# Performance work log

Measured on AMD Instinct MI355X. Metric: run time of the kernel, lower is better.

Reference implementation:

```python
import jax, jax.numpy as jnp
import numpy as np

VOCAB = 50257
HIDDEN = 2048
BATCH = 8
SEQ = 2048
TOPK = 256


def setup_inputs() -> dict:
    key = jax.random.key(0)
    k1, k2 = jax.random.split(key)
    input_ids = jax.random.randint(k1, (BATCH, SEQ), 0, VOCAB, dtype=jnp.int64)
    W = jax.random.normal(k2, (VOCAB, HIDDEN), dtype=jnp.float32)
    return {"input_ids": input_ids, "W": W, "k": TOPK}


def reference(input_ids, W, k):
    # Embedding gather: [B, S] ids -> [B, S, H] logits (irregular row gather).
    logits = jnp.take(W, input_ids, axis=0)
    # Top-k over the last (hidden) dim, sorted descending (matches torch.topk).
    values, indices = jax.lax.top_k(logits, k)
    return values, indices.astype(jnp.int32)
```

## Files before the change

### kernel.cpp

```cpp
#include <hip/hip_runtime.h>
#include <stdint.h>

#define VOCAB  50257
#define HIDDEN 2048
#define NTOK   (8 * 2048)
#define TOPK   256
#define WPB    4


__device__ __forceinline__ void cmpex(uint64_t& a, uint64_t& b, bool desc) {
    bool gt = a > b;
    uint64_t mx = gt ? a : b;
    uint64_t mn = gt ? b : a;
    a = desc ? mx : mn;
    b = desc ? mn : mx;
}

__device__ __forceinline__ void step_xor(uint64_t& v, int r, int lane, int lx, int k) {
    uint64_t p = __shfl_xor(v, lx, 64);
    int i = lane * 4 + r;
    bool desc = ((i & k) == 0);
    bool low  = ((lane & lx) == 0);
    bool keep_max = (desc == low);
    bool gt = v > p;
    v = (keep_max == gt) ? v : p;
}

__global__ __launch_bounds__(256) void topk_kernel(
    const int* __restrict__ ids,
    const float* __restrict__ W,
    float* __restrict__ out)
{
    const int lane = threadIdx.x & 63;
    const int w    = threadIdx.x >> 6;
    const int row  = blockIdx.x * WPB + w;

    __shared__ __align__(16) uint64_t sel[WPB][256];

    const int id = ids[row];
    const float4* src = (const float4*)(W + (size_t)id * HIDDEN);

    uint32_t sv[32];
#pragma unroll
    for (int c = 0; c < 8; ++c) {
        float4 v = src[c * 64 + lane];
        uint32_t u[4] = {__float_as_uint(v.x), __float_as_uint(v.y),
                         __float_as_uint(v.z), __float_as_uint(v.w)};
#pragma unroll
        for (int j = 0; j < 4; ++j) {
            uint32_t m = (u[j] & 0x80000000u) ? 0xFFFFFFFFu : 0x80000000u;
            sv[c * 4 + j] = u[j] ^ m;
        }
    }

    auto count_ge = [&](uint32_t T) -> uint32_t {
        uint32_t tot = 0;
#pragma unroll
        for (int e = 0; e < 32; ++e)
            tot += (uint32_t)__popcll(__ballot(sv[e] >= T));
        return tot;
    };

    uint32_t lo = 0u, hi = 0xFFFFFFFFu;
    uint32_t Tsel = 0u;
    bool exact = false;
    while (lo < hi) {
        uint32_t mid = lo + ((hi - lo) >> 1) + 1u;
        uint32_t c = count_ge(mid);
        if (c == TOPK) { Tsel = mid; exact = true; break; }
        if (c > TOPK) lo = mid; else hi = mid - 1u;
    }

    uint32_t selmask = 0u;
    if (exact) {
#pragma unroll
        for (int e = 0; e < 32; ++e)
            if (sv[e] >= Tsel) selmask |= (1u << e);
    } else {
        uint32_t vstar = lo;
        uint32_t m = (vstar == 0xFFFFFFFFu) ? 0u : count_ge(vstar + 1u);
        uint32_t r = TOPK - m;
        const uint64_t below = (1ull << lane) - 1ull;
        uint32_t base = 0u;
        for (int c = 0; c < 8; ++c) {
            uint64_t bj[4];
            uint32_t pre = 0u;
#pragma unroll
            for (int j = 0; j < 4; ++j) {
                bj[j] = __ballot(sv[c * 4 + j] == vstar);
                pre += (uint32_t)__popcll(bj[j] & below);
            }
            uint32_t ownpref = 0u;
#pragma unroll
            for (int j = 0; j < 4; ++j) {
                int e = c * 4 + j;
                bool eq = (sv[e] == vstar);
                uint32_t rank = base + pre + ownpref;
                if (sv[e] > vstar || (eq && rank < r)) selmask |= (1u << e);
                ownpref += eq ? 1u : 0u;
            }
#pragma unroll
            for (int j = 0; j < 4; ++j)
                base += (uint32_t)__popcll(bj[j]);
        }
    }

    const uint64_t below = (1ull << lane) - 1ull;
    uint32_t pbase = 0u;
#pragma unroll
    for (int e = 0; e < 32; ++e) {
        bool s = (selmask >> e) & 1u;
        uint64_t mm = __ballot(s);
        if (s) {
            uint32_t idx = (uint32_t)((e >> 2) * 256 + lane * 4 + (e & 3));
            uint64_t kk = ((uint64_t)sv[e] << 16) | (uint64_t)(0xFFFFu ^ idx);
            uint32_t p = pbase + (uint32_t)__popcll(mm & below);
            sel[w][p] = kk;
        }
        pbase += (uint32_t)__popcll(mm);
    }
    __threadfence_block();

    uint64_t v0 = sel[w][lane * 4 + 0];
    uint64_t v1 = sel[w][lane * 4 + 1];
    uint64_t v2 = sel[w][lane * 4 + 2];
    uint64_t v3 = sel[w][lane * 4 + 3];

#pragma unroll
    for (int k = 2; k <= 256; k <<= 1) {
#pragma unroll
        for (int j = 128; j >= 4; j >>= 1) {
            if (j <= (k >> 1)) {
                int lx = j >> 2;
                step_xor(v0, 0, lane, lx, k);
                step_xor(v1, 1, lane, lx, k);
                step_xor(v2, 2, lane, lx, k);
                step_xor(v3, 3, lane, lx, k);
            }
        }
        if (k >= 4) {
            bool d02 = (((lane * 4 + 0) & k) == 0);
            bool d13 = (((lane * 4 + 1) & k) == 0);
            cmpex(v0, v2, d02);
            cmpex(v1, v3, d13);
        }
        bool d01 = (((lane * 4 + 0) & k) == 0);
        bool d23 = (((lane * 4 + 2) & k) == 0);
        cmpex(v0, v1, d01);
        cmpex(v2, v3, d23);
    }

    uint64_t kk[4] = {v0, v1, v2, v3};
    float ov[4], oi[4];
#pragma unroll
    for (int r = 0; r < 4; ++r) {
        uint32_t s = (uint32_t)(kk[r] >> 16);
        ov[r] = __uint_as_float((s & 0x80000000u) ? (s & 0x7FFFFFFFu) : ~s);
        oi[r] = (float)(0xFFFFu ^ (uint32_t)(kk[r] & 0xFFFFu));
    }
    float4* out_v = (float4*)(out + (size_t)row * TOPK);
    float4* out_i = (float4*)(out + (size_t)NTOK * TOPK + (size_t)row * TOPK);
    out_v[lane] = make_float4(ov[0], ov[1], ov[2], ov[3]);
    out_i[lane] = make_float4(oi[0], oi[1], oi[2], oi[3]);
}

extern "C" void kernel_launch(void* const* d_in, const int* in_sizes, int n_in,
                              void* d_out, int out_size, void* d_ws, size_t ws_size,
                              hipStream_t stream) {
    const int*   ids = (const int*)d_in[0];
    const float* W   = (const float*)d_in[1];
    float* out = (float*)d_out;

    topk_kernel<<<NTOK / WPB, 256, 0, stream>>>(ids, W, out);
}
```

Measured before the change: 514.7 us.

## Narrow radix-select bounds and use DPP wave reductions for counting and compaction

Each lane tracks its top-4 values during the load, and wave min/max of these give tight initial bounds for the threshold binary search, so fewer iterations are needed. Per-iteration counting now does a per-lane count plus a DPP scan reduction instead of 32 ballots with popcount. Compaction into shared memory uses one per-lane prefix scan over the selected count instead of 32 ballots. This cuts cross-lane operations per search step but adds min/max work per element during the load. The lower bound relies on the 256th value being at least the smallest of the per-lane 4th maxima, which holds since 64 lanes times 4 is 256.

```diff
diff --git a/kernel.cpp b/kernel.cpp
--- a/kernel.cpp
+++ b/kernel.cpp
@@ -7,6 +7,40 @@
 #define TOPK   256
 #define WPB    4
 
+
+__device__ __forceinline__ uint32_t umax32(uint32_t a, uint32_t b) { return a > b ? a : b; }
+__device__ __forceinline__ uint32_t umin32(uint32_t a, uint32_t b) { return a < b ? a : b; }
+
+__device__ __forceinline__ uint32_t scan_add(uint32_t v) {
+    v += (uint32_t)__builtin_amdgcn_update_dpp(0, (int)v, 0x111, 0xf, 0xf, false);
+    v += (uint32_t)__builtin_amdgcn_update_dpp(0, (int)v, 0x112, 0xf, 0xf, false);
+    v += (uint32_t)__builtin_amdgcn_update_dpp(0, (int)v, 0x114, 0xf, 0xf, false);
+    v += (uint32_t)__builtin_amdgcn_update_dpp(0, (int)v, 0x118, 0xf, 0xf, false);
+    v += (uint32_t)__builtin_amdgcn_update_dpp(0, (int)v, 0x142, 0xa, 0xf, false);
+    v += (uint32_t)__builtin_amdgcn_update_dpp(0, (int)v, 0x143, 0xc, 0xf, false);
+    return v;
+}
+__device__ __forceinline__ uint32_t wave_sum(uint32_t v) {
+    return (uint32_t)__builtin_amdgcn_readlane((int)scan_add(v), 63);
+}
+__device__ __forceinline__ uint32_t wave_max(uint32_t v) {
+    v = umax32(v, (uint32_t)__builtin_amdgcn_update_dpp(0, (int)v, 0x111, 0xf, 0xf, false));
+    v = umax32(v, (uint32_t)__builtin_amdgcn_update_dpp(0, (int)v, 0x112, 0xf, 0xf, false));
+    v = umax32(v, (uint32_t)__builtin_amdgcn_update_dpp(0, (int)v, 0x114, 0xf, 0xf, false));
+    v = umax32(v, (uint32_t)__builtin_amdgcn_update_dpp(0, (int)v, 0x118, 0xf, 0xf, false));
+    v = umax32(v, (uint32_t)__builtin_amdgcn_update_dpp(0, (int)v, 0x142, 0xa, 0xf, false));
+    v = umax32(v, (uint32_t)__builtin_amdgcn_update_dpp(0, (int)v, 0x143, 0xc, 0xf, false));
+    return (uint32_t)__builtin_amdgcn_readlane((int)v, 63);
+}
+__device__ __forceinline__ uint32_t wave_min(uint32_t v) {
+    v = umin32(v, (uint32_t)__builtin_amdgcn_update_dpp(-1, (int)v, 0x111, 0xf, 0xf, false));
+    v = umin32(v, (uint32_t)__builtin_amdgcn_update_dpp(-1, (int)v, 0x112, 0xf, 0xf, false));
+    v = umin32(v, (uint32_t)__builtin_amdgcn_update_dpp(-1, (int)v, 0x114, 0xf, 0xf, false));
+    v = umin32(v, (uint32_t)__builtin_amdgcn_update_dpp(-1, (int)v, 0x118, 0xf, 0xf, false));
+    v = umin32(v, (uint32_t)__builtin_amdgcn_update_dpp(-1, (int)v, 0x142, 0xa, 0xf, false));
+    v = umin32(v, (uint32_t)__builtin_amdgcn_update_dpp(-1, (int)v, 0x143, 0xc, 0xf, false));
+    return (uint32_t)__builtin_amdgcn_readlane((int)v, 63);
+}
 
 __device__ __forceinline__ void cmpex(uint64_t& a, uint64_t& b, bool desc) {
     bool gt = a > b;
@@ -41,6 +75,7 @@
     const float4* src = (const float4*)(W + (size_t)id * HIDDEN);
 
     uint32_t sv[32];
+    uint32_t m0 = 0u, m1 = 0u, m2 = 0u, m3 = 0u;
 #pragma unroll
     for (int c = 0; c < 8; ++c) {
         float4 v = src[c * 64 + lane];
@@ -49,19 +84,26 @@
 #pragma unroll
         for (int j = 0; j < 4; ++j) {
             uint32_t m = (u[j] & 0x80000000u) ? 0xFFFFFFFFu : 0x80000000u;
-            sv[c * 4 + j] = u[j] ^ m;
-        }
-    }
+            uint32_t s = u[j] ^ m;
+            sv[c * 4 + j] = s;
+            uint32_t b0 = umin32(m0, s);  m0 = umax32(m0, s);
+            uint32_t b1 = umin32(m1, b0); m1 = umax32(m1, b0);
+            uint32_t b2 = umin32(m2, b1); m2 = umax32(m2, b1);
+            m3 = umax32(m3, b2);
+        }
+    }
+
+    uint32_t lo = wave_min(m3);
+    uint32_t hi = wave_max(m0);
 
     auto count_ge = [&](uint32_t T) -> uint32_t {
-        uint32_t tot = 0;
+        uint32_t c = 0u;
 #pragma unroll
         for (int e = 0; e < 32; ++e)
-            tot += (uint32_t)__popcll(__ballot(sv[e] >= T));
-        return tot;
+            c += (sv[e] >= T) ? 1u : 0u;
+        return wave_sum(c);
     };
 
-    uint32_t lo = 0u, hi = 0xFFFFFFFFu;
     uint32_t Tsel = 0u;
     bool exact = false;
     while (lo < hi) {
@@ -105,19 +147,16 @@
         }
     }
 
-    const uint64_t below = (1ull << lane) - 1ull;
-    uint32_t pbase = 0u;
+    uint32_t nsel = (uint32_t)__popc(selmask);
+    uint32_t pos  = scan_add(nsel) - nsel;
+    const int lane4 = lane * 4;
 #pragma unroll
     for (int e = 0; e < 32; ++e) {
-        bool s = (selmask >> e) & 1u;
-        uint64_t mm = __ballot(s);
-        if (s) {
-            uint32_t idx = (uint32_t)((e >> 2) * 256 + lane * 4 + (e & 3));
-            uint64_t kk = ((uint64_t)sv[e] << 16) | (uint64_t)(0xFFFFu ^ idx);
-            uint32_t p = pbase + (uint32_t)__popcll(mm & below);
-            sel[w][p] = kk;
-        }
-        pbase += (uint32_t)__popcll(mm);
+        if ((selmask >> e) & 1u) {
+            uint32_t idx = (uint32_t)((e >> 2) * 256 + lane4 + (e & 3));
+            sel[w][pos] = ((uint64_t)sv[e] << 16) | (uint64_t)(0xFFFFu ^ idx);
+            pos++;
+        }
     }
     __threadfence_block();
 
```

After: 504.3 us. 1.02x faster.
